# Performance work log

Measured on AMD Instinct MI355X. Metric: run time of the kernel, lower is better.

Reference implementation:

```python
import jax, jax.numpy as jnp
import numpy as np

T = 2048          # tokens (flattened prefill)
H = 3584          # hidden_size
NH = 16           # num query heads
NKV = 8           # num kv heads
G = NH // NKV     # GQA group size
D = 256           # head_dim
SCALE = 256.0 ** -0.5   # query_pre_attn_scalar ** -0.5
WINDOW = 1024     # sliding_window_size
CAP = 50.0        # logit softcap
BASE = 10000.0    # rope theta
NEG = -1e30


def _rope(x, positions):
    # x: [T, n, D], neox-style rotary over full head_dim
    half = D // 2
    inv_freq = 1.0 / (BASE ** (jnp.arange(0, D, 2, dtype=jnp.float32) / D))  # [half]
    ang = positions.astype(jnp.float32)[:, None] * inv_freq  # [T, half]
    cos = jnp.cos(ang)[:, None, :]  # [T,1,half]
    sin = jnp.sin(ang)[:, None, :]
    x1, x2 = x[..., :half], x[..., half:]
    return jnp.concatenate([x1 * cos - x2 * sin, x2 * cos + x1 * sin], axis=-1)


def setup_inputs() -> dict:
    key = jax.random.key(0)
    ks = jax.random.split(key, 5)
    s = 0.02
    return {
        "hidden_states": jax.random.normal(ks[0], (T, H), dtype=jnp.float32),
        "Wq": jax.random.normal(ks[1], (H, NH * D), dtype=jnp.float32) * s,
        "Wk": jax.random.normal(ks[2], (H, NKV * D), dtype=jnp.float32) * s,
        "Wv": jax.random.normal(ks[3], (H, NKV * D), dtype=jnp.float32) * s,
        "Wo": jax.random.normal(ks[4], (NH * D, H), dtype=jnp.float32) * s,
        "positions": jnp.arange(T, dtype=jnp.int32),
    }


def reference(hidden_states, Wq, Wk, Wv, Wo, positions):
    q = (hidden_states @ Wq).reshape(T, NH, D)
    k = (hidden_states @ Wk).reshape(T, NKV, D)
    v = (hidden_states @ Wv).reshape(T, NKV, D)
    q = _rope(q, positions)
    k = _rope(k, positions)

    # GQA attention: group query heads over kv heads
    qg = (q * SCALE).reshape(T, NKV, G, D)
    scores = jnp.einsum('qhgd,khd->hgqk', qg, k)  # [NKV,G,T,T]
    scores = CAP * jnp.tanh(scores / CAP)         # logit softcap

    i = jnp.arange(T)[:, None]
    j = jnp.arange(T)[None, :]
    mask = (j <= i) & (i - j < WINDOW)            # causal + sliding window
    scores = jnp.where(mask, scores, NEG)

    p = jax.nn.softmax(scores, axis=-1)
    o = jnp.einsum('hgqk,khd->qhgd', p, v).reshape(T, NH * D)
    return o @ Wo
```

## Files before the change

kernel.cpp:

```cpp
#include <hip/hip_runtime.h>
#include <math.h>

typedef __attribute__((ext_vector_type(8))) __bf16 bf16x8;
typedef __attribute__((ext_vector_type(4))) __bf16 bf16x4;
typedef __attribute__((ext_vector_type(4))) float f32x4;

#define TSEQ 2048
#define HDIM 3584
#define NQH  16
#define NKVH 8
#define DH   256
#define WIN  1024
#define QKD  (NQH * DH)
#define KVD  (NKVH * DH)
#define QKVN 8192

#define MFMA __builtin_amdgcn_mfma_f32_16x16x32_bf16

__device__ __forceinline__ void gload_lds16(const void* g, void* l) {
  __builtin_amdgcn_global_load_lds(
      (const __attribute__((address_space(1))) void*)g,
      (__attribute__((address_space(3))) void*)l, 16, 0, 0);
}


__global__ void cvt_bf16_kernel(const float* __restrict__ in,
                                __bf16* __restrict__ out, long n) {
  long i = ((long)blockIdx.x * blockDim.x + threadIdx.x) * 4;
  if (i >= n) return;
  float4 v = *reinterpret_cast<const float4*>(in + i);
  bf16x4 o4;
  o4.x = (__bf16)v.x; o4.y = (__bf16)v.y; o4.z = (__bf16)v.z; o4.w = (__bf16)v.w;
  *reinterpret_cast<bf16x4*>(out + i) = o4;
}

__global__ void transpose_cvt_kernel(const float* __restrict__ in,
                                     __bf16* __restrict__ out, int R, int C) {
  __shared__ float tile[32][33];
  const int tx = threadIdx.x, ty = threadIdx.y;
  const int c0 = blockIdx.x * 32, r0 = blockIdx.y * 32;
#pragma unroll
  for (int i = 0; i < 4; ++i)
    tile[ty + i * 8][tx] = in[(size_t)(r0 + ty + i * 8) * C + (c0 + tx)];
  __syncthreads();
#pragma unroll
  for (int i = 0; i < 4; ++i)
    out[(size_t)(c0 + ty + i * 8) * R + (r0 + tx)] = (__bf16)tile[tx][ty + i * 8];
}

__global__ void transpose_bf16_kernel(const __bf16* __restrict__ in,
                                      __bf16* __restrict__ out, int ldin, int ldout) {
  __shared__ __bf16 tile[32][33];
  const int tx = threadIdx.x, ty = threadIdx.y;
  const int c0 = blockIdx.x * 32, r0 = blockIdx.y * 32;
#pragma unroll
  for (int i = 0; i < 4; ++i)
    tile[ty + i * 8][tx] = in[(size_t)(r0 + ty + i * 8) * ldin + (c0 + tx)];
  __syncthreads();
#pragma unroll
  for (int i = 0; i < 4; ++i)
    out[(size_t)(c0 + ty + i * 8) * ldout + (r0 + tx)] = tile[tx][ty + i * 8];
}

__global__ void rope_table_kernel(const int* __restrict__ positions,
                                  float* __restrict__ ct,
                                  float* __restrict__ st) {
  int i = blockIdx.x * blockDim.x + threadIdx.x;
  if (i >= TSEQ * 128) return;
  int t = i >> 7, j = i & 127;
  float invf = (float)exp((double)(-2 * j) * (9.210340371976184 / 256.0));
  float ang = (float)positions[t] * invf;
  ct[i] = cosf(ang);
  st[i] = sinf(ang);
}

__global__ void rope_apply_kernel(__bf16* __restrict__ x,
                                  const float* __restrict__ ct,
                                  const float* __restrict__ st,
                                  int heads, int ld, float scale, int total) {
  int i = blockIdx.x * blockDim.x + threadIdx.x;
  if (i >= total) return;
  int j = i & 127;
  int th = i >> 7;
  int t = th / heads;
  int head = th - t * heads;
  size_t base = (size_t)t * ld + head * DH + j;
  float x1 = (float)x[base], x2 = (float)x[base + 128];
  float c = ct[(t << 7) + j], s = st[(t << 7) + j];
  x[base]       = (__bf16)((x1 * c - x2 * s) * scale);
  x[base + 128] = (__bf16)((x2 * c + x1 * s) * scale);
}

__global__ void reduce2_kernel(const float* __restrict__ p0,
                               const float* __restrict__ p1,
                               float* __restrict__ out, int n4) {
  int stride = gridDim.x * blockDim.x;
  for (int i = blockIdx.x * blockDim.x + threadIdx.x; i < n4; i += stride) {
    float4 a = reinterpret_cast<const float4*>(p0)[i];
    float4 b = reinterpret_cast<const float4*>(p1)[i];
    a.x += b.x; a.y += b.y; a.z += b.z; a.w += b.w;
    reinterpret_cast<float4*>(out)[i] = a;
  }
}


__device__ __forceinline__ void stage_half(const __bf16* __restrict__ gbase,
                                           int row0, int ldg, int k0,
                                           __bf16* lds_half, int tid) {
  const int lane = tid & 63;
  const int w = tid >> 6;
  const int lr = lane >> 3;
  const int swzcol = ((lane & 7) ^ lr) << 3;
  const __bf16* g = gbase + (size_t)(row0 + w * 8 + lr) * ldg + k0 + swzcol;
  __bf16* l = lds_half + w * 512;
  gload_lds16(g, l);
  gload_lds16(g + (size_t)64 * ldg, l + 4096);
}

template <typename CT>
__global__ __launch_bounds__(512, 2) void gemm256_kernel(
    const __bf16* __restrict__ A, const __bf16* __restrict__ B,
    CT* __restrict__ C, int lda, int Klen, int ldc, int nrc, size_t cstride) {
  __shared__ __bf16 lds[2][2][2][8192];

  const int nwg = gridDim.x;
  const int per = nwg >> 3;
  const int wg = (blockIdx.x & 7) * per + (blockIdx.x >> 3);
  const int kslice = wg / nrc;
  const int rem = wg - kslice * nrc;
  const int row0 = (rem & 7) * 256;
  const int col0 = (rem >> 3) * 256;
  const int k0 = kslice * Klen;
  CT* Cs = C + (size_t)kslice * cstride;

  const int tid = threadIdx.x;
  const int lane = tid & 63, w = tid >> 6;
  const int wr = w >> 2, wc = w & 3;
  const int l15 = lane & 15, lg = lane >> 4;
  const int swz = (lane & 7) << 3;
  const int kxa = (lg * 8) ^ swz;
  const int kxb = (32 + lg * 8) ^ swz;
  const int bro = (wc & 1) * 64;

  const __bf16* Ablk = A + (size_t)row0 * lda + k0;
  const __bf16* Bblk = B + (size_t)col0 * lda + k0;

  f32x4 acc[8][4] = {};
  const int NT = Klen >> 6;

  stage_half(Ablk, 0,   lda, 0,  &lds[0][0][0][0], tid);
  stage_half(Ablk, 128, lda, 0,  &lds[0][0][1][0], tid);
  stage_half(Bblk, 0,   lda, 0,  &lds[0][1][0][0], tid);
  stage_half(Bblk, 128, lda, 0,  &lds[0][1][1][0], tid);
  stage_half(Ablk, 0,   lda, 64, &lds[1][0][0][0], tid);
  stage_half(Ablk, 128, lda, 64, &lds[1][0][1][0], tid);
  asm volatile("s_waitcnt vmcnt(4)" ::: "memory");
  __builtin_amdgcn_s_barrier();

  for (int t = 0; t < NT; ++t) {
    const int cur = t & 1, nxt = cur ^ 1;
    const __bf16* Ah = &lds[cur][0][wr][0];
    const __bf16* Bh = &lds[cur][1][wc >> 1][0];

    bf16x8 a[8][2], b[4][2];
#pragma unroll
    for (int m = 0; m < 8; ++m) {
      const __bf16* p = Ah + (m * 16 + l15) * 64;
      a[m][0] = *(const bf16x8*)(p + kxa);
      a[m][1] = *(const bf16x8*)(p + kxb);
    }
#pragma unroll
    for (int n = 0; n < 4; ++n) {
      const __bf16* p = Bh + (bro + n * 16 + l15) * 64;
      b[n][0] = *(const bf16x8*)(p + kxa);
      b[n][1] = *(const bf16x8*)(p + kxb);
    }

    if (t + 1 < NT) {
      stage_half(Bblk, 0,   lda, (t + 1) * 64, &lds[nxt][1][0][0], tid);
      stage_half(Bblk, 128, lda, (t + 1) * 64, &lds[nxt][1][1][0], tid);
    }

    asm volatile("s_waitcnt lgkmcnt(0)" ::: "memory");
    __builtin_amdgcn_s_barrier();
    if (t + 2 < NT) {
      stage_half(Ablk, 0,   lda, (t + 2) * 64, &lds[cur][0][0][0], tid);
      stage_half(Ablk, 128, lda, (t + 2) * 64, &lds[cur][0][1][0], tid);
    }

    __builtin_amdgcn_s_setprio(1);
#pragma unroll
    for (int m = 0; m < 8; ++m)
#pragma unroll
      for (int n = 0; n < 4; ++n) {
        acc[m][n] = MFMA(a[m][0], b[n][0], acc[m][n], 0, 0, 0);
        acc[m][n] = MFMA(a[m][1], b[n][1], acc[m][n], 0, 0, 0);
      }
    __builtin_amdgcn_s_setprio(0);

    if (t + 2 < NT) {
      asm volatile("s_waitcnt vmcnt(4)" ::: "memory");
    } else {
      asm volatile("s_waitcnt vmcnt(0)" ::: "memory");
    }
    __builtin_amdgcn_s_barrier();
  }

#pragma unroll
  for (int m = 0; m < 8; ++m)
#pragma unroll
    for (int n = 0; n < 4; ++n)
#pragma unroll
      for (int r = 0; r < 4; ++r) {
        int row = row0 + wr * 128 + m * 16 + lg * 4 + r;
        int col = col0 + wc * 64 + n * 16 + l15;
        Cs[(size_t)row * ldc + col] = (CT)acc[m][n][r];
      }
}

__global__ __launch_bounds__(256, 2) void attn_kernel(
    const __bf16* __restrict__ q, const __bf16* __restrict__ k,
    const __bf16* __restrict__ vt, __bf16* __restrict__ o) {
  __shared__ __bf16 Klds[64][264];
  __shared__ __bf16 Vlds[256][72];
  __shared__ __bf16 Plds[4][16][72];

  const int tid = threadIdx.x;
  const int wave = tid >> 6;
  const int lane = tid & 63;
  const int l16 = lane & 15;
  const int lg = lane >> 4;
  const int qh = blockIdx.y;
  const int h = qh >> 1;
  const int q0 = blockIdx.x << 6;
  const int qr = q0 + wave * 16;

  bf16x8 qf[8];
  {
    const __bf16* qp = q + (size_t)(qr + l16) * QKVN + qh * DH + lg * 8;
#pragma unroll
    for (int ds = 0; ds < 8; ++ds)
      qf[ds] = *reinterpret_cast<const bf16x8*>(qp + ds * 32);
  }

  f32x4 accO[16] = {};
  float m_run[4] = {-1e30f, -1e30f, -1e30f, -1e30f};
  float l_run[4] = {0.f, 0.f, 0.f, 0.f};

  int t_lo = q0 - (WIN - 1);
  if (t_lo < 0) t_lo = 0;
  t_lo &= ~63;

  for (int t0 = t_lo; t0 <= q0; t0 += 64) {
    __syncthreads();
    {
      const __bf16* kg = k + (size_t)t0 * QKVN + h * DH;
#pragma unroll
      for (int it = 0; it < 8; ++it) {
        int c = tid + it * 256;
        int row = c >> 5, col = (c & 31) * 8;
        *reinterpret_cast<bf16x8*>(&Klds[row][col]) =
            *reinterpret_cast<const bf16x8*>(kg + (size_t)row * QKVN + col);
      }
      const __bf16* vg = vt + (size_t)(h * DH) * TSEQ + t0;
#pragma unroll
      for (int it = 0; it < 8; ++it) {
        int c = tid + it * 256;
        int row = c >> 3, col = (c & 7) * 8;
        *reinterpret_cast<bf16x8*>(&Vlds[row][col]) =
            *reinterpret_cast<const bf16x8*>(vg + (size_t)row * TSEQ + col);
      }
    }
    __syncthreads();

    f32x4 accS[4] = {};
#pragma unroll
    for (int nt = 0; nt < 4; ++nt)
#pragma unroll
      for (int ds = 0; ds < 8; ++ds) {
        bf16x8 kf = *reinterpret_cast<const bf16x8*>(&Klds[nt * 16 + l16][ds * 32 + lg * 8]);
        accS[nt] = MFMA(qf[ds], kf, accS[nt], 0, 0, 0);
      }

    float pv[4][4];
    float mt[4] = {-1e30f, -1e30f, -1e30f, -1e30f};
#pragma unroll
    for (int nt = 0; nt < 4; ++nt) {
      int key = t0 + nt * 16 + l16;
#pragma unroll
      for (int r = 0; r < 4; ++r) {
        int row = qr + lg * 4 + r;
        float s = 50.f * tanhf(accS[nt][r] * 0.02f);
        bool valid = (key <= row) && (row - key < WIN);
        s = valid ? s : -1e30f;
        pv[nt][r] = s;
        mt[r] = fmaxf(mt[r], s);
      }
    }
#pragma unroll
    for (int off = 1; off < 16; off <<= 1)
#pragma unroll
      for (int r = 0; r < 4; ++r)
        mt[r] = fmaxf(mt[r], __shfl_xor(mt[r], off));

    float rs[4];
#pragma unroll
    for (int r = 0; r < 4; ++r) {
      float mn = fmaxf(m_run[r], mt[r]);
      float sc = __expf(m_run[r] - mn);
      m_run[r] = mn;
      l_run[r] *= sc;
      float s0 = 0.f;
#pragma unroll
      for (int nt = 0; nt < 4; ++nt) {
        float p = (pv[nt][r] > -1e29f) ? __expf(pv[nt][r] - mn) : 0.f;
        pv[nt][r] = p;
        s0 += p;
      }
      rs[r] = s0;
#pragma unroll
      for (int nt2 = 0; nt2 < 16; ++nt2)
        accO[nt2][r] *= sc;
    }
#pragma unroll
    for (int off = 1; off < 16; off <<= 1)
#pragma unroll
      for (int r = 0; r < 4; ++r)
        rs[r] += __shfl_xor(rs[r], off);
#pragma unroll
    for (int r = 0; r < 4; ++r)
      l_run[r] += rs[r];

#pragma unroll
    for (int nt = 0; nt < 4; ++nt)
#pragma unroll
      for (int r = 0; r < 4; ++r)
        Plds[wave][lg * 4 + r][nt * 16 + l16] = (__bf16)pv[nt][r];

#pragma unroll
    for (int ks = 0; ks < 2; ++ks) {
      bf16x8 pa = *reinterpret_cast<const bf16x8*>(&Plds[wave][l16][ks * 32 + lg * 8]);
#pragma unroll
      for (int nt2 = 0; nt2 < 16; ++nt2) {
        bf16x8 vb = *reinterpret_cast<const bf16x8*>(&Vlds[nt2 * 16 + l16][ks * 32 + lg * 8]);
        accO[nt2] = MFMA(pa, vb, accO[nt2], 0, 0, 0);
      }
    }
  }

#pragma unroll
  for (int r = 0; r < 4; ++r) {
    float inv_l = 1.f / l_run[r];
    int row = qr + lg * 4 + r;
#pragma unroll
    for (int nt2 = 0; nt2 < 16; ++nt2)
      o[(size_t)row * QKD + qh * DH + nt2 * 16 + l16] = (__bf16)(accO[nt2][r] * inv_l);
  }
}


extern "C" void kernel_launch(void* const* d_in, const int* in_sizes, int n_in,
                              void* d_out, int out_size, void* d_ws, size_t ws_size,
                              hipStream_t stream) {
  const float* hs = (const float*)d_in[0];
  const float* Wq = (const float*)d_in[1];
  const float* Wk = (const float*)d_in[2];
  const float* Wv = (const float*)d_in[3];
  const float* Wo = (const float*)d_in[4];
  const int* positions = (const int*)d_in[5];
  float* out = (float*)d_out;

  char* ws = (char*)d_ws;
  const size_t SZ_HS  = (size_t)TSEQ * HDIM * 2;
  const size_t SZ_WQT = (size_t)QKD * HDIM * 2;
  const size_t SZ_WKT = (size_t)KVD * HDIM * 2;
  const size_t SZ_WOT = (size_t)HDIM * QKD * 2;
  const size_t SZ_QKV = (size_t)TSEQ * QKVN * 2;
  const size_t SZ_O   = (size_t)TSEQ * QKD * 2;
  const size_t SZ_TBL = (size_t)TSEQ * 128 * 4;

  __bf16* hs_bf = (__bf16*)ws; ws += SZ_HS;
  __bf16* WqT   = (__bf16*)ws; ws += SZ_WQT;
  __bf16* WkT   = (__bf16*)ws; ws += SZ_WKT;
  __bf16* WvT   = (__bf16*)ws; ws += SZ_WKT;
  __bf16* WoT   = (__bf16*)ws; ws += SZ_WOT;
  __bf16* qkv   = (__bf16*)ws; ws += SZ_QKV;
  __bf16* o_bf  = (__bf16*)ws; ws += SZ_O;
  float*  cost  = (float*)ws;  ws += SZ_TBL;
  float*  sint  = (float*)ws;  ws += SZ_TBL;
  __bf16* vt_bf = hs_bf;
  float* cpart = (float*)WqT;
  if ((size_t)(ws - (char*)d_ws) > ws_size) return;

  cvt_bf16_kernel<<<(TSEQ * HDIM) / 1024, 256, 0, stream>>>(hs, hs_bf, (long)TSEQ * HDIM);
  transpose_cvt_kernel<<<dim3(QKD / 32, HDIM / 32), dim3(32, 8), 0, stream>>>(Wq, WqT, HDIM, QKD);
  transpose_cvt_kernel<<<dim3(KVD / 32, HDIM / 32), dim3(32, 8), 0, stream>>>(Wk, WkT, HDIM, KVD);
  transpose_cvt_kernel<<<dim3(KVD / 32, HDIM / 32), dim3(32, 8), 0, stream>>>(Wv, WvT, HDIM, KVD);
  transpose_cvt_kernel<<<dim3(HDIM / 32, QKD / 32), dim3(32, 8), 0, stream>>>(Wo, WoT, QKD, HDIM);
  rope_table_kernel<<<(TSEQ * 128) / 256, 256, 0, stream>>>(positions, cost, sint);

  gemm256_kernel<__bf16><<<256, 512, 0, stream>>>(hs_bf, WqT, qkv, HDIM, HDIM, QKVN, 256, 0);

  rope_apply_kernel<<<(TSEQ * NQH * 128) / 256, 256, 0, stream>>>(qkv, cost, sint, NQH, QKVN, 0.0625f, TSEQ * NQH * 128);
  rope_apply_kernel<<<(TSEQ * NKVH * 128) / 256, 256, 0, stream>>>(qkv + QKD, cost, sint, NKVH, QKVN, 1.0f, TSEQ * NKVH * 128);
  transpose_bf16_kernel<<<dim3(KVD / 32, TSEQ / 32), dim3(32, 8), 0, stream>>>(qkv + QKD + KVD, vt_bf, QKVN, TSEQ);

  attn_kernel<<<dim3(TSEQ / 64, NQH), 256, 0, stream>>>(qkv, qkv + QKD, vt_bf, o_bf);

  gemm256_kernel<float><<<224, 512, 0, stream>>>(o_bf, WoT, cpart, QKD, QKD / 2, HDIM, 112,
                                                 (size_t)TSEQ * HDIM);
  reduce2_kernel<<<1792, 256, 0, stream>>>(cpart, cpart + (size_t)TSEQ * HDIM, out,
                                           TSEQ * HDIM / 4);
}
```

Baseline: 354.9 us.

## Unroll GEMM into quadrant phases and drop online-softmax max tracking

The GEMM main loop is unrolled by two. Each k-step is split into four MFMA quadrants with barriers between them, and global-to-LDS staging is interleaved between the quadrants so loads overlap with compute. The attention kernel drops the running max and the rescaling of accumulators. It relies on the softcap bounding logits to ±50, computes exp(softcap(s) - 50) directly as exp(-100/(exp(0.04 s)+1)), and adds s_setprio around the MFMA blocks. This removes the max shuffles and the per-tile accumulator rescale. The risk is a loss of precision when all logits are far below the cap, since the probabilities become tiny relative to exp(0).

```diff
diff --git a/kernel.cpp b/kernel.cpp
--- a/kernel.cpp
+++ b/kernel.cpp
@@ -117,6 +117,37 @@
   gload_lds16(g + (size_t)64 * ldg, l + 4096);
 }
 
+#define BAR __builtin_amdgcn_s_barrier()
+
+#define RD_A(DST, BASE, MO)                                         \
+  _Pragma("unroll")                                                 \
+  for (int m_ = 0; m_ < 4; ++m_) {                                  \
+    const __bf16* p_ = (BASE) + (((MO) + m_) * 16 + l15) * 64;      \
+    DST[m_][0] = *(const bf16x8*)(p_ + kxa);                        \
+    DST[m_][1] = *(const bf16x8*)(p_ + kxb);                        \
+  }
+
+#define RD_B(DST, BASE, NO)                                         \
+  _Pragma("unroll")                                                 \
+  for (int n_ = 0; n_ < 2; ++n_) {                                  \
+    const __bf16* p_ = (BASE) + (bro + ((NO) + n_) * 16 + l15) * 64;\
+    DST[n_][0] = *(const bf16x8*)(p_ + kxa);                        \
+    DST[n_][1] = *(const bf16x8*)(p_ + kxb);                        \
+  }
+
+#define MQUAD(AF, BF, MO, NO)                                          \
+  __builtin_amdgcn_s_setprio(1);                                       \
+  _Pragma("unroll")                                                    \
+  for (int m_ = 0; m_ < 4; ++m_)                                       \
+    _Pragma("unroll")                                                  \
+    for (int n_ = 0; n_ < 2; ++n_) {                                   \
+      acc[(MO) + m_][(NO) + n_] =                                      \
+          MFMA(AF[m_][0], BF[n_][0], acc[(MO) + m_][(NO) + n_], 0, 0, 0); \
+      acc[(MO) + m_][(NO) + n_] =                                      \
+          MFMA(AF[m_][1], BF[n_][1], acc[(MO) + m_][(NO) + n_], 0, 0, 0); \
+    }                                                                  \
+  __builtin_amdgcn_s_setprio(0);
+
 template <typename CT>
 __global__ __launch_bounds__(512, 2) void gemm256_kernel(
     const __bf16* __restrict__ A, const __bf16* __restrict__ B,
@@ -145,8 +176,14 @@
   const __bf16* Ablk = A + (size_t)row0 * lda + k0;
   const __bf16* Bblk = B + (size_t)col0 * lda + k0;
 
+  const __bf16* Ae = &lds[0][0][wr][0];
+  const __bf16* Be = &lds[0][1][wc >> 1][0];
+  const __bf16* Ao = &lds[1][0][wr][0];
+  const __bf16* Bo = &lds[1][1][wc >> 1][0];
+
   f32x4 acc[8][4] = {};
   const int NT = Klen >> 6;
+  const int NI = NT >> 1;
 
   stage_half(Ablk, 0,   lda, 0,  &lds[0][0][0][0], tid);
   stage_half(Ablk, 128, lda, 0,  &lds[0][0][1][0], tid);
@@ -155,55 +192,55 @@
   stage_half(Ablk, 0,   lda, 64, &lds[1][0][0][0], tid);
   stage_half(Ablk, 128, lda, 64, &lds[1][0][1][0], tid);
   asm volatile("s_waitcnt vmcnt(4)" ::: "memory");
-  __builtin_amdgcn_s_barrier();
-
-  for (int t = 0; t < NT; ++t) {
-    const int cur = t & 1, nxt = cur ^ 1;
-    const __bf16* Ah = &lds[cur][0][wr][0];
-    const __bf16* Bh = &lds[cur][1][wc >> 1][0];
-
-    bf16x8 a[8][2], b[4][2];
-#pragma unroll
-    for (int m = 0; m < 8; ++m) {
-      const __bf16* p = Ah + (m * 16 + l15) * 64;
-      a[m][0] = *(const bf16x8*)(p + kxa);
-      a[m][1] = *(const bf16x8*)(p + kxb);
-    }
-#pragma unroll
-    for (int n = 0; n < 4; ++n) {
-      const __bf16* p = Bh + (bro + n * 16 + l15) * 64;
-      b[n][0] = *(const bf16x8*)(p + kxa);
-      b[n][1] = *(const bf16x8*)(p + kxb);
-    }
-
-    if (t + 1 < NT) {
-      stage_half(Bblk, 0,   lda, (t + 1) * 64, &lds[nxt][1][0][0], tid);
-      stage_half(Bblk, 128, lda, (t + 1) * 64, &lds[nxt][1][1][0], tid);
-    }
-
-    asm volatile("s_waitcnt lgkmcnt(0)" ::: "memory");
-    __builtin_amdgcn_s_barrier();
-    if (t + 2 < NT) {
-      stage_half(Ablk, 0,   lda, (t + 2) * 64, &lds[cur][0][0][0], tid);
-      stage_half(Ablk, 128, lda, (t + 2) * 64, &lds[cur][0][1][0], tid);
-    }
-
-    __builtin_amdgcn_s_setprio(1);
-#pragma unroll
-    for (int m = 0; m < 8; ++m)
-#pragma unroll
-      for (int n = 0; n < 4; ++n) {
-        acc[m][n] = MFMA(a[m][0], b[n][0], acc[m][n], 0, 0, 0);
-        acc[m][n] = MFMA(a[m][1], b[n][1], acc[m][n], 0, 0, 0);
-      }
-    __builtin_amdgcn_s_setprio(0);
-
-    if (t + 2 < NT) {
+  BAR;
+
+  bf16x8 a03[4][2], a47[4][2], b01[2][2], b23[2][2];
+
+  for (int j = 0; j < NI; ++j) {
+    const int e = 2 * j, o = 2 * j + 1;
+    const bool last = (j == NI - 1);
+
+    RD_A(a03, Ae, 0);
+    RD_B(b01, Be, 0);
+    stage_half(Bblk, 0, lda, o * 64, &lds[1][1][0][0], tid);
+    asm volatile("s_waitcnt lgkmcnt(8)" ::: "memory");
+    BAR; MQUAD(a03, b01, 0, 0); BAR;
+
+    RD_A(a47, Ae, 4);
+    stage_half(Bblk, 128, lda, o * 64, &lds[1][1][1][0], tid);
+    BAR; MQUAD(a47, b01, 4, 0); BAR;
+
+    RD_B(b23, Be, 2);
+    if (!last) stage_half(Ablk, 0, lda, (e + 2) * 64, &lds[0][0][0][0], tid);
+    BAR; MQUAD(a47, b23, 4, 2); BAR;
+
+    if (!last) {
+      stage_half(Ablk, 128, lda, (e + 2) * 64, &lds[0][0][1][0], tid);
       asm volatile("s_waitcnt vmcnt(4)" ::: "memory");
     } else {
       asm volatile("s_waitcnt vmcnt(0)" ::: "memory");
     }
-    __builtin_amdgcn_s_barrier();
+    BAR; MQUAD(a03, b23, 0, 2); BAR;
+
+    RD_A(a03, Ao, 0);
+    RD_B(b01, Bo, 0);
+    if (!last) stage_half(Bblk, 0, lda, (e + 2) * 64, &lds[0][1][0][0], tid);
+    asm volatile("s_waitcnt lgkmcnt(8)" ::: "memory");
+    BAR; MQUAD(a03, b01, 0, 0); BAR;
+
+    RD_A(a47, Ao, 4);
+    if (!last) stage_half(Bblk, 128, lda, (e + 2) * 64, &lds[0][1][1][0], tid);
+    BAR; MQUAD(a47, b01, 4, 0); BAR;
+
+    RD_B(b23, Bo, 2);
+    if (!last) stage_half(Ablk, 0, lda, (o + 2) * 64, &lds[1][0][0][0], tid);
+    BAR; MQUAD(a47, b23, 4, 2); BAR;
+
+    if (!last) {
+      stage_half(Ablk, 128, lda, (o + 2) * 64, &lds[1][0][1][0], tid);
+      asm volatile("s_waitcnt vmcnt(4)" ::: "memory");
+    }
+    BAR; MQUAD(a03, b23, 0, 2); BAR;
   }
 
 #pragma unroll
@@ -244,7 +281,6 @@
   }
 
   f32x4 accO[16] = {};
-  float m_run[4] = {-1e30f, -1e30f, -1e30f, -1e30f};
   float l_run[4] = {0.f, 0.f, 0.f, 0.f};
 
   int t_lo = q0 - (WIN - 1);
@@ -274,6 +310,7 @@
     __syncthreads();
 
     f32x4 accS[4] = {};
+    __builtin_amdgcn_s_setprio(1);
 #pragma unroll
     for (int nt = 0; nt < 4; ++nt)
 #pragma unroll
@@ -281,46 +318,22 @@
         bf16x8 kf = *reinterpret_cast<const bf16x8*>(&Klds[nt * 16 + l16][ds * 32 + lg * 8]);
         accS[nt] = MFMA(qf[ds], kf, accS[nt], 0, 0, 0);
       }
-
-    float pv[4][4];
-    float mt[4] = {-1e30f, -1e30f, -1e30f, -1e30f};
+    __builtin_amdgcn_s_setprio(0);
+
+    float rs[4] = {0.f, 0.f, 0.f, 0.f};
 #pragma unroll
     for (int nt = 0; nt < 4; ++nt) {
       int key = t0 + nt * 16 + l16;
 #pragma unroll
       for (int r = 0; r < 4; ++r) {
         int row = qr + lg * 4 + r;
-        float s = 50.f * tanhf(accS[nt][r] * 0.02f);
+        float t = __expf(accS[nt][r] * 0.04f);
+        float p = __expf(-100.0f / (t + 1.0f));
         bool valid = (key <= row) && (row - key < WIN);
-        s = valid ? s : -1e30f;
-        pv[nt][r] = s;
-        mt[r] = fmaxf(mt[r], s);
-      }
-    }
-#pragma unroll
-    for (int off = 1; off < 16; off <<= 1)
-#pragma unroll
-      for (int r = 0; r < 4; ++r)
-        mt[r] = fmaxf(mt[r], __shfl_xor(mt[r], off));
-
-    float rs[4];
-#pragma unroll
-    for (int r = 0; r < 4; ++r) {
-      float mn = fmaxf(m_run[r], mt[r]);
-      float sc = __expf(m_run[r] - mn);
-      m_run[r] = mn;
-      l_run[r] *= sc;
-      float s0 = 0.f;
-#pragma unroll
-      for (int nt = 0; nt < 4; ++nt) {
-        float p = (pv[nt][r] > -1e29f) ? __expf(pv[nt][r] - mn) : 0.f;
-        pv[nt][r] = p;
-        s0 += p;
-      }
-      rs[r] = s0;
-#pragma unroll
-      for (int nt2 = 0; nt2 < 16; ++nt2)
-        accO[nt2][r] *= sc;
+        p = valid ? p : 0.f;
+        rs[r] += p;
+        Plds[wave][lg * 4 + r][nt * 16 + l16] = (__bf16)p;
+      }
     }
 #pragma unroll
     for (int off = 1; off < 16; off <<= 1)
@@ -331,12 +344,7 @@
     for (int r = 0; r < 4; ++r)
       l_run[r] += rs[r];
 
-#pragma unroll
-    for (int nt = 0; nt < 4; ++nt)
-#pragma unroll
-      for (int r = 0; r < 4; ++r)
-        Plds[wave][lg * 4 + r][nt * 16 + l16] = (__bf16)pv[nt][r];
-
+    __builtin_amdgcn_s_setprio(1);
 #pragma unroll
     for (int ks = 0; ks < 2; ++ks) {
       bf16x8 pa = *reinterpret_cast<const bf16x8*>(&Plds[wave][l16][ks * 32 + lg * 8]);
@@ -346,6 +354,7 @@
         accO[nt2] = MFMA(pa, vb, accO[nt2], 0, 0, 0);
       }
     }
+    __builtin_amdgcn_s_setprio(0);
   }
 
 #pragma unroll
```

Measured after the change: 340.5 us. 1.04x faster.
